# Kernel tuning notes

Measured on AMD Instinct MI355X. Metric: run time of the kernel, lower is better.

## Reference

```python
import jax, jax.numpy as jnp
import numpy as np

B, C, H, W = 8, 512, 64, 64
RED = 8
D = C // RED  # query/key channels


def setup_inputs() -> dict:
    key = jax.random.key(0)
    ks = jax.random.split(key, 5)
    skip = jax.random.normal(ks[0], (B, C, H, W), dtype=jnp.float32)
    res = jax.random.normal(ks[1], (B, C, H, W), dtype=jnp.float32)
    # 1x1 Conv1d weights (no bias). Spectral norm is a weight parametrization;
    # these tensors represent the effective (normalized) weights at forward time.
    Wq = jax.random.normal(ks[2], (D, C), dtype=jnp.float32) * 0.02
    Wk = jax.random.normal(ks[3], (D, C), dtype=jnp.float32) * 0.02
    Wv = jax.random.normal(ks[4], (C, C), dtype=jnp.float32) * 0.02
    gamma = jnp.asarray([0.5], dtype=jnp.float32)  # nonzero so attention branch contributes
    return {"skip": skip, "res": res, "Wq": Wq, "Wk": Wk, "Wv": Wv, "gamma": gamma}


def reference(skip, res, Wq, Wk, Wv, gamma):
    b, c, h, w = skip.shape
    n = h * w
    x_skip = skip.reshape(b, c, n)  # [B, C, N]
    x_res = res.reshape(b, c, n)
    # 1x1 convs == per-position matmuls
    f = jnp.einsum('dc,bcn->bdn', Wq, x_skip)  # [B, D, N]
    g = jnp.einsum('dc,bcn->bdn', Wk, x_skip)  # [B, D, N]
    hv = jnp.einsum('oc,bcn->bon', Wv, x_res)  # [B, C, N]
    # scores[b, i, j] = sum_d f[b, d, i] * g[b, d, j]; softmax over dim=1 (the i axis)
    scores = jnp.einsum('bdi,bdj->bij', f, g)  # [B, N, N]
    beta = jax.nn.softmax(scores, axis=1)
    o = gamma * jnp.einsum('bci,bij->bcj', hv, beta) + x_skip  # [B, C, N]
    return o.reshape(b, c, h, w)
```

## Files before the change

### kernel.cpp

```cpp
#include <hip/hip_runtime.h>


#define B_ 8
#define C_ 512
#define N_ 4096
#define D_ 64

typedef __bf16 bf16x8 __attribute__((ext_vector_type(8)));
typedef float  f32x16 __attribute__((ext_vector_type(16)));

#define MFMA32 __builtin_amdgcn_mfma_f32_32x32x16_bf16

__device__ __forceinline__ unsigned pk_bf16(float a, float b) {
  unsigned r;
  asm("v_cvt_pk_bf16_f32 %0, %1, %2" : "=v"(r) : "v"(a), "v"(b));
  return r;
}

__device__ __forceinline__ bf16x8 ldg_frag(const unsigned short* p) {
  uint4 u = *(const uint4*)p;
  return __builtin_bit_cast(bf16x8, u);
}
__device__ __forceinline__ bf16x8 lds_frag(const unsigned char* p) {
  uint4 u = *(const uint4*)p;
  return __builtin_bit_cast(bf16x8, u);
}

__global__ void cvt_w(const float* __restrict__ src, unsigned short* __restrict__ dst, int n) {
  int i = (blockIdx.x * blockDim.x + threadIdx.x) * 2;
  if (i + 1 < n + 1) {
    unsigned v = pk_bf16(src[i], src[i + 1]);
    *(unsigned*)(dst + i) = v;
  }
}

__device__ __forceinline__ void stage64(const float* __restrict__ src,
                                        unsigned char* __restrict__ dst, int t) {
  int si = (t & 15) << 2;
  int cl = (t >> 4) << 1;
#pragma unroll
  for (int p = 0; p < 2; ++p) {
    int c = cl + p * 32;
    const float* r0 = src + (size_t)c * N_ + si;
    float4 a0 = *(const float4*)r0;
    float4 a1 = *(const float4*)(r0 + N_);
    const float* f0 = (const float*)&a0;
    const float* f1 = (const float*)&a1;
    int cb = c << 1;
#pragma unroll
    for (int k = 0; k < 4; ++k) {
      int ii = si + k;
      unsigned v = pk_bf16(f0[k], f1[k]);
      *(unsigned*)(dst + (((ii << 7) + cb) ^ ((ii & 7) << 4))) = v;
    }
  }
}

__global__ __launch_bounds__(256, 2) void fg_proj(
    const float* __restrict__ skip,
    const unsigned short* __restrict__ Wqb, const unsigned short* __restrict__ Wkb,
    unsigned short* __restrict__ Kmat, unsigned short* __restrict__ Qmat) {
  __shared__ __align__(16) unsigned char Xs[2][8192];
  int blk = blockIdx.x, b = blk & 7, i0 = (blk >> 3) << 6;
  int t = threadIdx.x, lane = t & 63, w = t >> 6, hi = lane >> 5, l5 = lane & 31;
  int dh = w >> 1, ih = w & 1;
  f32x16 ka, qa;
#pragma unroll
  for (int r = 0; r < 16; ++r) { ka[r] = 0.f; qa[r] = 0.f; }
  int il = (ih << 5) + l5;
  int dr = (dh << 5) + l5;
#pragma unroll 1
  for (int kk = 0; kk < 8; ++kk) {
    int c0 = kk << 6;
    unsigned char* buf = Xs[kk & 1];
    stage64(skip + ((size_t)(b * C_ + c0)) * N_ + i0, buf, t);
    __syncthreads();
#pragma unroll
    for (int ks = 0; ks < 4; ++ks) {
      int co = (ks << 4) + (hi << 3);
      bf16x8 aq = ldg_frag(Wqb + (size_t)dr * C_ + c0 + co);
      bf16x8 ak = ldg_frag(Wkb + (size_t)dr * C_ + c0 + co);
      bf16x8 bx = lds_frag(buf + (((il << 7) + (co << 1)) ^ ((il & 7) << 4)));
      ka = MFMA32(aq, bx, ka, 0, 0, 0);
      qa = MFMA32(ak, bx, qa, 0, 0, 0);
    }
  }
  size_t rowb = ((size_t)b * N_ + i0 + il) * D_ + (dh << 5);
#pragma unroll
  for (int q = 0; q < 4; ++q) {
    int dq = (q << 3) + (hi << 2);
    uint2 v;
    v.x = pk_bf16(ka[q * 4 + 0], ka[q * 4 + 1]);
    v.y = pk_bf16(ka[q * 4 + 2], ka[q * 4 + 3]);
    *(uint2*)(Kmat + rowb + dq) = v;
    v.x = pk_bf16(qa[q * 4 + 0], qa[q * 4 + 1]);
    v.y = pk_bf16(qa[q * 4 + 2], qa[q * 4 + 3]);
    *(uint2*)(Qmat + rowb + dq) = v;
  }
}

__global__ __launch_bounds__(256, 2) void hv_proj(
    const float* __restrict__ res, const unsigned short* __restrict__ Wvb,
    unsigned short* __restrict__ Vmat) {
  __shared__ __align__(16) unsigned char Xs[2][8192];
  int blk = blockIdx.x, b = blk & 7, i0 = (blk >> 3) << 6;
  int t = threadIdx.x, lane = t & 63, w = t >> 6, hi = lane >> 5, l5 = lane & 31;
  int cw = w << 7;
  f32x16 acc[2][4];
#pragma unroll
  for (int a = 0; a < 2; ++a)
#pragma unroll
    for (int c = 0; c < 4; ++c)
#pragma unroll
      for (int r = 0; r < 16; ++r) acc[a][c][r] = 0.f;
#pragma unroll 1
  for (int kk = 0; kk < 8; ++kk) {
    int c0 = kk << 6;
    unsigned char* buf = Xs[kk & 1];
    stage64(res + ((size_t)(b * C_ + c0)) * N_ + i0, buf, t);
    __syncthreads();
#pragma unroll
    for (int ks = 0; ks < 4; ++ks) {
      int co = (ks << 4) + (hi << 3);
      bf16x8 a0 = lds_frag(buf + (((l5 << 7) + (co << 1)) ^ ((l5 & 7) << 4)));
      bf16x8 a1 = lds_frag(buf + ((((32 + l5) << 7) + (co << 1)) ^ ((l5 & 7) << 4)));
#pragma unroll
      for (int ct = 0; ct < 4; ++ct) {
        bf16x8 bv = ldg_frag(Wvb + (size_t)(cw + (ct << 5) + l5) * C_ + c0 + co);
        acc[0][ct] = MFMA32(a0, bv, acc[0][ct], 0, 0, 0);
        acc[1][ct] = MFMA32(a1, bv, acc[1][ct], 0, 0, 0);
      }
    }
  }
#pragma unroll
  for (int ihh = 0; ihh < 2; ++ihh)
#pragma unroll
    for (int ct = 0; ct < 4; ++ct) {
      int c = cw + (ct << 5) + l5;
      unsigned short* vp = Vmat + ((size_t)b * C_ + c) * N_ + i0 + (ihh << 5);
#pragma unroll
      for (int q = 0; q < 4; ++q) {
        int iq = (q << 3) + (hi << 2);
        uint2 v;
        v.x = pk_bf16(acc[ihh][ct][q * 4 + 0], acc[ihh][ct][q * 4 + 1]);
        v.y = pk_bf16(acc[ihh][ct][q * 4 + 2], acc[ihh][ct][q * 4 + 3]);
        *(uint2*)(vp + iq) = v;
      }
    }
}

__device__ __forceinline__ void online_upd(float& m, float& l, const f32x16& s) {
  float t0 = fmaxf(s[0], s[1]),  t1 = fmaxf(s[2], s[3]);
  float t2 = fmaxf(s[4], s[5]),  t3 = fmaxf(s[6], s[7]);
  float t4 = fmaxf(s[8], s[9]),  t5 = fmaxf(s[10], s[11]);
  float t6 = fmaxf(s[12], s[13]), t7 = fmaxf(s[14], s[15]);
  t0 = fmaxf(t0, t1); t2 = fmaxf(t2, t3); t4 = fmaxf(t4, t5); t6 = fmaxf(t6, t7);
  float tm = fmaxf(fmaxf(t0, t2), fmaxf(t4, t6));
  float nm = fmaxf(m, tm);
  float a0 = l * __expf(m - nm), a1 = 0.f;
#pragma unroll
  for (int r = 0; r < 16; r += 2) {
    a0 += __expf(s[r] - nm);
    a1 += __expf(s[r + 1] - nm);
  }
  m = nm;
  l = a0 + a1;
}

__global__ __launch_bounds__(512) void stats_k(
    const unsigned short* __restrict__ Kmat, const unsigned short* __restrict__ Qmat,
    const float* __restrict__ gamma, float* __restrict__ m_ws, float* __restrict__ sc_ws) {
  __shared__ float mr[8][64];
  __shared__ float lr[8][64];
  int blk = blockIdx.x, b = blk & 7, j0 = (blk >> 3) << 6;
  int t = threadIdx.x, lane = t & 63, w = t >> 6, hi = lane >> 5, l5 = lane & 31;
  bf16x8 qf[2][4];
#pragma unroll
  for (int jh = 0; jh < 2; ++jh)
#pragma unroll
    for (int ks = 0; ks < 4; ++ks)
      qf[jh][ks] = ldg_frag(Qmat + ((size_t)b * N_ + j0 + (jh << 5) + l5) * D_ + (ks << 4) + (hi << 3));
  float m0 = -INFINITY, l0 = 0.f, m1 = -INFINITY, l1 = 0.f;
  for (int it = w; it < 128; it += 8) {
    const unsigned short* kp = Kmat + ((size_t)b * N_ + (it << 5) + l5) * D_ + (hi << 3);
    f32x16 s0, s1;
#pragma unroll
    for (int r = 0; r < 16; ++r) { s0[r] = 0.f; s1[r] = 0.f; }
#pragma unroll
    for (int ks = 0; ks < 4; ++ks) {
      bf16x8 a = ldg_frag(kp + (ks << 4));
      s0 = MFMA32(a, qf[0][ks], s0, 0, 0, 0);
      s1 = MFMA32(a, qf[1][ks], s1, 0, 0, 0);
    }
    online_upd(m0, l0, s0);
    online_upd(m1, l1, s1);
  }
  {
    float om = __shfl_xor(m0, 32);
    float ol = __shfl_xor(l0, 32);
    float nm = fmaxf(m0, om);
    l0 = l0 * __expf(m0 - nm) + ol * __expf(om - nm);
    m0 = nm;
    om = __shfl_xor(m1, 32);
    ol = __shfl_xor(l1, 32);
    nm = fmaxf(m1, om);
    l1 = l1 * __expf(m1 - nm) + ol * __expf(om - nm);
    m1 = nm;
  }
  mr[w][lane] = (lane < 32) ? m0 : m1;
  lr[w][lane] = (lane < 32) ? l0 : l1;
  __syncthreads();
  if (t < 64) {
    float M = mr[0][t];
#pragma unroll
    for (int ww = 1; ww < 8; ++ww) M = fmaxf(M, mr[ww][t]);
    float L = 0.f;
#pragma unroll
    for (int ww = 0; ww < 8; ++ww) L += lr[ww][t] * __expf(mr[ww][t] - M);
    m_ws[(size_t)b * N_ + j0 + t] = M;
    sc_ws[(size_t)b * N_ + j0 + t] = gamma[0] / L;
  }
}

__global__ __launch_bounds__(256, 3) void attn_pv(
    const unsigned short* __restrict__ Kmat, const unsigned short* __restrict__ Qmat,
    const unsigned short* __restrict__ Vmat, const float* __restrict__ m_ws,
    const float* __restrict__ sc_ws, const float* __restrict__ skip,
    float* __restrict__ out) {
  __shared__ __align__(16) unsigned char P[2][8192];
  int blk = blockIdx.x, b = blk & 7, ch = (blk >> 3) & 1, j0 = (blk >> 4) << 6;
  int t = threadIdx.x, lane = t & 63, w = t >> 6, hi = lane >> 5, l5 = lane & 31;
  int ih = w >> 1, jh = w & 1;
  int cbase = (ch << 8) + (w << 6);
  bf16x8 qf[4];
#pragma unroll
  for (int ks = 0; ks < 4; ++ks)
    qf[ks] = ldg_frag(Qmat + ((size_t)b * N_ + j0 + (jh << 5) + l5) * D_ + (ks << 4) + (hi << 3));
  float mj = m_ws[(size_t)b * N_ + j0 + (jh << 5) + l5];
  float scj = sc_ws[(size_t)b * N_ + j0 + (jh << 5) + l5];
  f32x16 acc[2][2];
#pragma unroll
  for (int a = 0; a < 2; ++a)
#pragma unroll
    for (int c = 0; c < 2; ++c)
#pragma unroll
      for (int r = 0; r < 16; ++r) acc[a][c][r] = 0.f;
  int jw = (jh << 5) + l5;
  unsigned wbase = jw << 7;
  unsigned wswz = (jw & 7) << 4;
  const unsigned short* Vb = Vmat + ((size_t)b * C_ + cbase + l5) * N_ + (hi << 3);
  const unsigned short* Kb = Kmat + ((size_t)b * N_ + (ih << 5) + l5) * D_ + (hi << 3);
#pragma unroll 1
  for (int it = 0; it < 64; ++it) {
    int ib = it << 6;
    unsigned char* pb = P[it & 1];
    bf16x8 vf[2][4];
#pragma unroll
    for (int ct = 0; ct < 2; ++ct)
#pragma unroll
      for (int ks = 0; ks < 4; ++ks)
        vf[ct][ks] = ldg_frag(Vb + (size_t)(ct << 5) * N_ + ib + (ks << 4));
    const unsigned short* kp = Kb + (size_t)ib * D_;
    f32x16 s;
#pragma unroll
    for (int r = 0; r < 16; ++r) s[r] = 0.f;
#pragma unroll
    for (int ks = 0; ks < 4; ++ks) {
      bf16x8 a = ldg_frag(kp + (ks << 4));
      s = MFMA32(a, qf[ks], s, 0, 0, 0);
    }
#pragma unroll
    for (int q = 0; q < 4; ++q) {
      float e0 = __expf(s[4 * q + 0] - mj) * scj;
      float e1 = __expf(s[4 * q + 1] - mj) * scj;
      float e2 = __expf(s[4 * q + 2] - mj) * scj;
      float e3 = __expf(s[4 * q + 3] - mj) * scj;
      uint2 v;
      v.x = pk_bf16(e0, e1);
      v.y = pk_bf16(e2, e3);
      int il = (ih << 5) + (q << 3) + (hi << 2);
      *(uint2*)(pb + ((wbase + (il << 1)) ^ wswz)) = v;
    }
    __syncthreads();
#pragma unroll
    for (int ks = 0; ks < 4; ++ks) {
      int iob = ((ks << 4) + (hi << 3)) << 1;
      bf16x8 pa0 = lds_frag(pb + (((l5 << 7) + iob) ^ ((l5 & 7) << 4)));
      bf16x8 pa1 = lds_frag(pb + ((((32 + l5) << 7) + iob) ^ ((l5 & 7) << 4)));
#pragma unroll
      for (int ct = 0; ct < 2; ++ct) {
        acc[0][ct] = MFMA32(pa0, vf[ct][ks], acc[0][ct], 0, 0, 0);
        acc[1][ct] = MFMA32(pa1, vf[ct][ks], acc[1][ct], 0, 0, 0);
      }
    }
  }
#pragma unroll
  for (int jt = 0; jt < 2; ++jt)
#pragma unroll
    for (int ct = 0; ct < 2; ++ct) {
      int c = cbase + (ct << 5) + l5;
      size_t base = ((size_t)b * C_ + c) * N_ + j0 + (jt << 5) + (hi << 2);
#pragma unroll
      for (int q = 0; q < 4; ++q) {
        float4 s4 = *(const float4*)(skip + base + (q << 3));
        float4 o4;
        o4.x = acc[jt][ct][q * 4 + 0] + s4.x;
        o4.y = acc[jt][ct][q * 4 + 1] + s4.y;
        o4.z = acc[jt][ct][q * 4 + 2] + s4.z;
        o4.w = acc[jt][ct][q * 4 + 3] + s4.w;
        *(float4*)(out + base + (q << 3)) = o4;
      }
    }
}

extern "C" void kernel_launch(void* const* d_in, const int* in_sizes, int n_in,
                              void* d_out, int out_size, void* d_ws, size_t ws_size,
                              hipStream_t stream) {
  (void)in_sizes; (void)n_in; (void)out_size; (void)ws_size;
  const float* skip = (const float*)d_in[0];
  const float* res = (const float*)d_in[1];
  const float* Wq = (const float*)d_in[2];
  const float* Wk = (const float*)d_in[3];
  const float* Wv = (const float*)d_in[4];
  const float* gamma = (const float*)d_in[5];
  float* out = (float*)d_out;
  char* ws = (char*)d_ws;

  unsigned short* Kmat = (unsigned short*)(ws);
  unsigned short* Qmat = (unsigned short*)(ws + (4ull << 20));
  unsigned short* Vmat = (unsigned short*)(ws + (8ull << 20));
  float* m_ws = (float*)(ws + (40ull << 20));
  float* sc_ws = (float*)(ws + (40ull << 20) + (128ull << 10));
  unsigned short* Wqb = (unsigned short*)(ws + (40ull << 20) + (256ull << 10));
  unsigned short* Wkb = Wqb + 64 * 512;
  unsigned short* Wvb = Wkb + 64 * 512;

  cvt_w<<<64, 256, 0, stream>>>(Wq, Wqb, 64 * 512);
  cvt_w<<<64, 256, 0, stream>>>(Wk, Wkb, 64 * 512);
  cvt_w<<<512, 256, 0, stream>>>(Wv, Wvb, 512 * 512);
  fg_proj<<<512, 256, 0, stream>>>(skip, Wqb, Wkb, Kmat, Qmat);
  hv_proj<<<512, 256, 0, stream>>>(res, Wvb, Vmat);
  stats_k<<<512, 512, 0, stream>>>(Kmat, Qmat, gamma, m_ws, sc_ws);
  attn_pv<<<1024, 256, 0, stream>>>(Kmat, Qmat, Vmat, m_ws, sc_ws, skip, out);
}
```

Baseline: 619.4 us.

## Keep P in registers via permlane32 swap, dropping LDS and block sync

Restructures attn_pv so each wave computes the scores for its own 32 keys against both 32-query halves. The exponentiated probabilities are repacked into MFMA A-operand layout with v_permlane32_swap instead of going through shared memory with a __syncthreads. Each block now covers all 512 channels (128 per wave), which halves the grid and removes the duplicate QK^T recomputation across channel halves. The exp is rewritten as exp2 with a folded scale. The costs are more accumulator registers (launch bounds drop to 2 blocks per CU) and fewer, larger blocks.

```diff
diff --git a/kernel.cpp b/kernel.cpp
--- a/kernel.cpp
+++ b/kernel.cpp
@@ -10,6 +10,8 @@
 typedef float  f32x16 __attribute__((ext_vector_type(16)));
 
 #define MFMA32 __builtin_amdgcn_mfma_f32_32x32x16_bf16
+#define L2E 1.4426950408889634f
+#define EXP2(x) __builtin_amdgcn_exp2f(x)
 
 __device__ __forceinline__ unsigned pk_bf16(float a, float b) {
   unsigned r;
@@ -222,92 +224,106 @@
   }
 }
 
-__global__ __launch_bounds__(256, 3) void attn_pv(
+__device__ __forceinline__ bf16x8 pack_p_slice(const float* s8, float nm, float sc) {
+  float e[8];
+#pragma unroll
+  for (int k = 0; k < 8; ++k) e[k] = EXP2(fmaf(s8[k], L2E, nm)) * sc;
+  unsigned w0 = pk_bf16(e[0], e[1]);
+  unsigned w1 = pk_bf16(e[2], e[3]);
+  unsigned w2 = pk_bf16(e[4], e[5]);
+  unsigned w3 = pk_bf16(e[6], e[7]);
+  asm("v_permlane32_swap_b32 %0, %1" : "+v"(w0), "+v"(w2));
+  asm("v_permlane32_swap_b32 %0, %1" : "+v"(w1), "+v"(w3));
+  uint4 u = {w0, w1, w2, w3};
+  return __builtin_bit_cast(bf16x8, u);
+}
+
+__global__ __launch_bounds__(256, 2) void attn_pv(
     const unsigned short* __restrict__ Kmat, const unsigned short* __restrict__ Qmat,
     const unsigned short* __restrict__ Vmat, const float* __restrict__ m_ws,
     const float* __restrict__ sc_ws, const float* __restrict__ skip,
     float* __restrict__ out) {
-  __shared__ __align__(16) unsigned char P[2][8192];
-  int blk = blockIdx.x, b = blk & 7, ch = (blk >> 3) & 1, j0 = (blk >> 4) << 6;
+  int blk = blockIdx.x, b = blk & 7, j0 = (blk >> 3) << 6;
   int t = threadIdx.x, lane = t & 63, w = t >> 6, hi = lane >> 5, l5 = lane & 31;
-  int ih = w >> 1, jh = w & 1;
-  int cbase = (ch << 8) + (w << 6);
-  bf16x8 qf[4];
-#pragma unroll
-  for (int ks = 0; ks < 4; ++ks)
-    qf[ks] = ldg_frag(Qmat + ((size_t)b * N_ + j0 + (jh << 5) + l5) * D_ + (ks << 4) + (hi << 3));
-  float mj = m_ws[(size_t)b * N_ + j0 + (jh << 5) + l5];
-  float scj = sc_ws[(size_t)b * N_ + j0 + (jh << 5) + l5];
-  f32x16 acc[2][2];
+  int cbase = w << 7;
+  bf16x8 qf[2][4];
+#pragma unroll
+  for (int jh = 0; jh < 2; ++jh)
+#pragma unroll
+    for (int ks = 0; ks < 4; ++ks)
+      qf[jh][ks] = ldg_frag(Qmat + ((size_t)b * N_ + j0 + (jh << 5) + l5) * D_ + (ks << 4) + (hi << 3));
+  float nm0 = -m_ws[(size_t)b * N_ + j0 + l5] * L2E;
+  float sc0 = sc_ws[(size_t)b * N_ + j0 + l5];
+  float nm1 = -m_ws[(size_t)b * N_ + j0 + 32 + l5] * L2E;
+  float sc1 = sc_ws[(size_t)b * N_ + j0 + 32 + l5];
+  f32x16 acc[2][4];
 #pragma unroll
   for (int a = 0; a < 2; ++a)
 #pragma unroll
-    for (int c = 0; c < 2; ++c)
+    for (int c = 0; c < 4; ++c)
 #pragma unroll
       for (int r = 0; r < 16; ++r) acc[a][c][r] = 0.f;
-  int jw = (jh << 5) + l5;
-  unsigned wbase = jw << 7;
-  unsigned wswz = (jw & 7) << 4;
-  const unsigned short* Vb = Vmat + ((size_t)b * C_ + cbase + l5) * N_ + (hi << 3);
-  const unsigned short* Kb = Kmat + ((size_t)b * N_ + (ih << 5) + l5) * D_ + (hi << 3);
+  const unsigned short* Kb = Kmat + ((size_t)b * N_ + l5) * D_ + (hi << 3);
+  const unsigned short* Vb = Vmat + ((size_t)(b * C_ + cbase + l5)) * N_ + (hi << 3);
 #pragma unroll 1
-  for (int it = 0; it < 64; ++it) {
-    int ib = it << 6;
-    unsigned char* pb = P[it & 1];
-    bf16x8 vf[2][4];
-#pragma unroll
-    for (int ct = 0; ct < 2; ++ct)
-#pragma unroll
-      for (int ks = 0; ks < 4; ++ks)
+  for (int it = 0; it < 128; ++it) {
+    int ib = it << 5;
+    bf16x8 kf[4];
+#pragma unroll
+    for (int ks = 0; ks < 4; ++ks)
+      kf[ks] = ldg_frag(Kb + (size_t)ib * D_ + (ks << 4));
+    bf16x8 vf[4][2];
+#pragma unroll
+    for (int ct = 0; ct < 4; ++ct)
+#pragma unroll
+      for (int ks = 0; ks < 2; ++ks)
         vf[ct][ks] = ldg_frag(Vb + (size_t)(ct << 5) * N_ + ib + (ks << 4));
-    const unsigned short* kp = Kb + (size_t)ib * D_;
-    f32x16 s;
-#pragma unroll
-    for (int r = 0; r < 16; ++r) s[r] = 0.f;
+    f32x16 s0, s1;
+#pragma unroll
+    for (int r = 0; r < 16; ++r) { s0[r] = 0.f; s1[r] = 0.f; }
 #pragma unroll
     for (int ks = 0; ks < 4; ++ks) {
-      bf16x8 a = ldg_frag(kp + (ks << 4));
-      s = MFMA32(a, qf[ks], s, 0, 0, 0);
-    }
-#pragma unroll
-    for (int q = 0; q < 4; ++q) {
-      float e0 = __expf(s[4 * q + 0] - mj) * scj;
-      float e1 = __expf(s[4 * q + 1] - mj) * scj;
-      float e2 = __expf(s[4 * q + 2] - mj) * scj;
-      float e3 = __expf(s[4 * q + 3] - mj) * scj;
-      uint2 v;
-      v.x = pk_bf16(e0, e1);
-      v.y = pk_bf16(e2, e3);
-      int il = (ih << 5) + (q << 3) + (hi << 2);
-      *(uint2*)(pb + ((wbase + (il << 1)) ^ wswz)) = v;
-    }
-    __syncthreads();
-#pragma unroll
-    for (int ks = 0; ks < 4; ++ks) {
-      int iob = ((ks << 4) + (hi << 3)) << 1;
-      bf16x8 pa0 = lds_frag(pb + (((l5 << 7) + iob) ^ ((l5 & 7) << 4)));
-      bf16x8 pa1 = lds_frag(pb + ((((32 + l5) << 7) + iob) ^ ((l5 & 7) << 4)));
-#pragma unroll
-      for (int ct = 0; ct < 2; ++ct) {
-        acc[0][ct] = MFMA32(pa0, vf[ct][ks], acc[0][ct], 0, 0, 0);
-        acc[1][ct] = MFMA32(pa1, vf[ct][ks], acc[1][ct], 0, 0, 0);
-      }
-    }
-  }
-#pragma unroll
-  for (int jt = 0; jt < 2; ++jt)
-#pragma unroll
-    for (int ct = 0; ct < 2; ++ct) {
+      s0 = MFMA32(kf[ks], qf[0][ks], s0, 0, 0, 0);
+      s1 = MFMA32(kf[ks], qf[1][ks], s1, 0, 0, 0);
+    }
+    bf16x8 pf0[2], pf1[2];
+    {
+      float sb[8];
+#pragma unroll
+      for (int ks = 0; ks < 2; ++ks) {
+#pragma unroll
+        for (int k = 0; k < 8; ++k) sb[k] = s0[8 * ks + k];
+        pf0[ks] = pack_p_slice(sb, nm0, sc0);
+      }
+#pragma unroll
+      for (int ks = 0; ks < 2; ++ks) {
+#pragma unroll
+        for (int k = 0; k < 8; ++k) sb[k] = s1[8 * ks + k];
+        pf1[ks] = pack_p_slice(sb, nm1, sc1);
+      }
+    }
+#pragma unroll
+    for (int ks = 0; ks < 2; ++ks)
+#pragma unroll
+      for (int ct = 0; ct < 4; ++ct) {
+        acc[0][ct] = MFMA32(pf0[ks], vf[ct][ks], acc[0][ct], 0, 0, 0);
+        acc[1][ct] = MFMA32(pf1[ks], vf[ct][ks], acc[1][ct], 0, 0, 0);
+      }
+  }
+#pragma unroll
+  for (int jh = 0; jh < 2; ++jh)
+#pragma unroll
+    for (int ct = 0; ct < 4; ++ct) {
       int c = cbase + (ct << 5) + l5;
-      size_t base = ((size_t)b * C_ + c) * N_ + j0 + (jt << 5) + (hi << 2);
+      size_t base = ((size_t)(b * C_ + c)) * N_ + j0 + (jh << 5) + (hi << 2);
 #pragma unroll
       for (int q = 0; q < 4; ++q) {
         float4 s4 = *(const float4*)(skip + base + (q << 3));
         float4 o4;
-        o4.x = acc[jt][ct][q * 4 + 0] + s4.x;
-        o4.y = acc[jt][ct][q * 4 + 1] + s4.y;
-        o4.z = acc[jt][ct][q * 4 + 2] + s4.z;
-        o4.w = acc[jt][ct][q * 4 + 3] + s4.w;
+        o4.x = acc[jh][ct][q * 4 + 0] + s4.x;
+        o4.y = acc[jh][ct][q * 4 + 1] + s4.y;
+        o4.z = acc[jh][ct][q * 4 + 2] + s4.z;
+        o4.w = acc[jh][ct][q * 4 + 3] + s4.w;
         *(float4*)(out + base + (q << 3)) = o4;
       }
     }
@@ -341,5 +357,5 @@
   fg_proj<<<512, 256, 0, stream>>>(skip, Wqb, Wkb, Kmat, Qmat);
   hv_proj<<<512, 256, 0, stream>>>(res, Wvb, Vmat);
   stats_k<<<512, 512, 0, stream>>>(Kmat, Qmat, gamma, m_ws, sc_ws);
-  attn_pv<<<1024, 256, 0, stream>>>(Kmat, Qmat, Vmat, m_ws, sc_ws, skip, out);
-}
+  attn_pv<<<512, 256, 0, stream>>>(Kmat, Qmat, Vmat, m_ws, sc_ws, skip, out);
+}
```

Result: no change. 624.0 us (+0.7%).
